# Optimization experiments

Measured on AMD Instinct MI355X. Metric: run time of the kernel, lower is better.

The kernel has to match this reference:

```python
import jax, jax.numpy as jnp
import numpy as np

N = 50000
E = 1600000
HID = 128
K = 2
EPS = 0.3


def setup_inputs() -> dict:
    key = jax.random.key(0)
    ks = jax.random.split(key, 8)
    x = jax.random.normal(ks[0], (N, 512), dtype=jnp.float32)
    edge_index = jax.random.randint(ks[1], (2, E), 0, N, dtype=jnp.int32)
    t1_w = jax.random.normal(ks[2], (HID, 512), dtype=jnp.float32) * (1.414 / np.sqrt(512))
    t1_b = jnp.zeros((HID,), dtype=jnp.float32)
    gate_w = jax.random.normal(ks[3], (K, 2 * HID), dtype=jnp.float32) * (1.414 / np.sqrt(2 * HID))
    gate_b = jnp.zeros((K,), dtype=jnp.float32)
    t2_w = jax.random.normal(ks[4], (40, HID), dtype=jnp.float32) * (1.414 / np.sqrt(HID))
    t2_b = jnp.zeros((40,), dtype=jnp.float32)
    return {"x": x, "edge_index": edge_index, "t1_w": t1_w, "t1_b": t1_b,
            "gate_w": gate_w, "gate_b": gate_b, "t2_w": t2_w, "t2_b": t2_b}


def reference(x, edge_index, t1_w, t1_b, gate_w, gate_b, t2_w, t2_b):
    row, col = edge_index[0], edge_index[1]
    # degree(row, num_nodes=N).clamp(min=1) ** -0.5
    deg = jax.ops.segment_sum(jnp.ones((E,), dtype=x.dtype), row, num_segments=N)
    norm_degree = jnp.clip(deg, 1.0) ** -0.5  # [N]

    h = jax.nn.relu(x @ t1_w.T + t1_b)  # [N, HID]
    raw = h
    for k in range(K):
        # gate(cat([h[row], h[col]], 1)) == h[row] @ W[:H] + h[col] @ W[H:]
        w_r, w_c = gate_w[k, :HID], gate_w[k, HID:]
        g = jnp.tanh(h[row] @ w_r + h[col] @ w_c + gate_b[k])  # [E]
        norm = g * norm_degree[row] * norm_degree[col]          # [E]
        # message: norm * x_j (x_j = h[row], source), scatter-add at col (target)
        agg = jax.ops.segment_sum(norm[:, None] * h[row], col, num_segments=N)
        h = EPS * raw + agg
    logits = h @ t2_w.T + t2_b  # [N, 40]
    return jax.nn.log_softmax(logits, axis=1)
```

## Files before the change

kernel.cpp:

```cpp
#include <hip/hip_runtime.h>
#include <hip/hip_bf16.h>
#include <hip/hip_fp16.h>

#define N_NODES 50000
#define N_EDGES 1600000
#define HIDDEN  128
#define EPS_C   0.3f
#define NWORDS  12500
#define CHUNK   12500
#define NCHUNK  128

typedef _Float16 f16x8 __attribute__((ext_vector_type(8)));
typedef _Float16 f16x4 __attribute__((ext_vector_type(4)));
typedef float    f32x16 __attribute__((ext_vector_type(16)));

__global__ __launch_bounds__(256) void k_hist(const int* __restrict__ ei, unsigned int* __restrict__ part) {
    __shared__ unsigned int hist[NWORDS];
    int b = blockIdx.x;
    int type  = b >> 7;
    int chunk = b & 127;
    const int* src = ei + (size_t)type * N_EDGES + (size_t)chunk * CHUNK;
    for (int i = threadIdx.x; i < NWORDS; i += 256) hist[i] = 0;
    __syncthreads();
    for (int i = threadIdx.x; i < CHUNK; i += 256) {
        int v = src[i];
        atomicAdd(&hist[v >> 2], 1u << ((v & 3) * 8));
    }
    __syncthreads();
    unsigned int* dst = part + ((size_t)type * NCHUNK + chunk) * NWORDS;
    for (int i = threadIdx.x; i < NWORDS; i += 256) dst[i] = hist[i];
}

__global__ __launch_bounds__(256) void k_reduce(const unsigned int* __restrict__ part,
                                                float* __restrict__ nd, int* __restrict__ cnt,
                                                unsigned short* __restrict__ cntpre) {
    int w = blockIdx.x * 256 + threadIdx.x;
    if (w >= NWORDS) return;
    unsigned int s0 = 0, s1 = 0, s2 = 0, s3 = 0;
    const unsigned int* dp = part + w;
    for (int b = 0; b < NCHUNK; ++b) {
        unsigned int v = dp[(size_t)b * NWORDS];
        s0 += v & 255u; s1 += (v >> 8) & 255u; s2 += (v >> 16) & 255u; s3 += v >> 24;
    }
    nd[4 * w + 0] = rsqrtf(fmaxf((float)s0, 1.f));
    nd[4 * w + 1] = rsqrtf(fmaxf((float)s1, 1.f));
    nd[4 * w + 2] = rsqrtf(fmaxf((float)s2, 1.f));
    nd[4 * w + 3] = rsqrtf(fmaxf((float)s3, 1.f));
    const unsigned int* cp = part + (size_t)NCHUNK * NWORDS + w;
    unsigned int r0 = 0, r1 = 0, r2 = 0, r3 = 0;
    for (int b = 0; b < NCHUNK; ++b) {
        size_t o = (size_t)b * N_NODES + 4 * w;
        *(ushort4*)&cntpre[o] = make_ushort4((unsigned short)r0, (unsigned short)r1,
                                             (unsigned short)r2, (unsigned short)r3);
        unsigned int v = cp[(size_t)b * NWORDS];
        r0 += v & 255u; r1 += (v >> 8) & 255u; r2 += (v >> 16) & 255u; r3 += v >> 24;
    }
    cnt[4 * w + 0] = (int)r0;
    cnt[4 * w + 1] = (int)r1;
    cnt[4 * w + 2] = (int)r2;
    cnt[4 * w + 3] = (int)r3;
}

__global__ __launch_bounds__(256) void k_scan_a(const int* __restrict__ cnt,
                                                int* __restrict__ out, int* __restrict__ partials) {
    __shared__ int sh[256];
    int t = threadIdx.x;
    int base = blockIdx.x * 1024 + t * 4;
    int v0 = (base + 0 < N_NODES) ? cnt[base + 0] : 0;
    int v1 = (base + 1 < N_NODES) ? cnt[base + 1] : 0;
    int v2 = (base + 2 < N_NODES) ? cnt[base + 2] : 0;
    int v3 = (base + 3 < N_NODES) ? cnt[base + 3] : 0;
    int s = v0 + v1 + v2 + v3;
    sh[t] = s;
    __syncthreads();
    for (int off = 1; off < 256; off <<= 1) {
        int add = (t >= off) ? sh[t - off] : 0;
        __syncthreads();
        sh[t] += add;
        __syncthreads();
    }
    int excl = sh[t] - s;
    if (t == 255) partials[blockIdx.x] = sh[255];
    if (base + 0 < N_NODES) out[base + 0] = excl;
    if (base + 1 < N_NODES) out[base + 1] = excl + v0;
    if (base + 2 < N_NODES) out[base + 2] = excl + v0 + v1;
    if (base + 3 < N_NODES) out[base + 3] = excl + v0 + v1 + v2;
}

__global__ void k_scan_b(int* partials, int* colptr, int nb) {
    if (threadIdx.x == 0 && blockIdx.x == 0) {
        int run = 0;
        for (int i = 0; i < nb; ++i) { int t = partials[i]; partials[i] = run; run += t; }
        colptr[N_NODES] = run;
    }
}

__global__ void k_scan_c(int* __restrict__ colptr, const int* __restrict__ partials) {
    int i = blockIdx.x * blockDim.x + threadIdx.x;
    if (i >= N_NODES) return;
    colptr[i] += partials[i >> 10];
}

__global__ __launch_bounds__(256) void k_scatter2(const int* __restrict__ ei, const int* __restrict__ colptr,
                                                  const unsigned short* __restrict__ cntpre,
                                                  int* __restrict__ csr) {
    __shared__ unsigned int rank[NWORDS];
    int b = blockIdx.x;
    for (int i = threadIdx.x; i < NWORDS; i += 256) rank[i] = 0;
    __syncthreads();
    const int* rs = ei + (size_t)b * CHUNK;
    const int* cs = ei + N_EDGES + (size_t)b * CHUNK;
    const unsigned short* pre = cntpre + (size_t)b * N_NODES;
    for (int i = threadIdx.x; i < CHUNK; i += 256) {
        int r = rs[i];
        int c = cs[i];
        unsigned int old = atomicAdd(&rank[c >> 2], 1u << ((c & 3) * 8));
        unsigned int lr = (old >> ((c & 3) * 8)) & 255u;
        int pos = colptr[c] + (int)pre[c] + (int)lr;
        csr[pos] = r;
    }
}

__global__ void k_cvt(const float4* __restrict__ src, __half2* __restrict__ dst, int n4) {
    int i = blockIdx.x * 256 + threadIdx.x;
    if (i >= n4) return;
    float4 v = src[i];
    dst[2 * i]     = __floats2half2_rn(v.x, v.y);
    dst[2 * i + 1] = __floats2half2_rn(v.z, v.w);
}

__global__ void k_cvtw(const float4* __restrict__ src, __half2* __restrict__ dst, int n4src, int n4tot) {
    int i = blockIdx.x * 256 + threadIdx.x;
    if (i >= n4tot) return;
    if (i < n4src) {
        float4 v = src[i];
        dst[2 * i]     = __floats2half2_rn(v.x, v.y);
        dst[2 * i + 1] = __floats2half2_rn(v.z, v.w);
    } else {
        __half2 z = __floats2half2_rn(0.f, 0.f);
        dst[2 * i]     = z;
        dst[2 * i + 1] = z;
    }
}

__global__ __launch_bounds__(256) void k_gemm1(const float* __restrict__ x, const _Float16* __restrict__ wh,
                                               const float* __restrict__ bias, _Float16* __restrict__ hb) {
    __shared__ _Float16 As[64 * 64];
    __shared__ _Float16 Bs[128 * 64];
    int t = threadIdx.x;
    int wave = t >> 6;
    int lane = t & 63;
    int lm   = lane & 31;
    int half = lane >> 5;
    int mstrip = wave & 1;
    int nstrip = wave >> 1;

    int m0  = blockIdx.x * 64;
    int wm0 = m0 + mstrip * 32;
    int n0  = nstrip * 64;

    int aidx[4], arow[4], ac4[4];
    int bidx, brow[4], bg[4];
#pragma unroll
    for (int i = 0; i < 4; ++i) {
        aidx[i] = i * 256 + t;
        arow[i] = aidx[i] >> 4;
        ac4[i]  = aidx[i] & 15;
        bidx    = i * 256 + t;
        brow[i] = bidx >> 3;
        bg[i]   = bidx & 7;
    }

    float4 pa[4];
    f16x8  pb[4];
#define LOAD_TILES(K0)                                                                    \
    {                                                                                     \
        _Pragma("unroll")                                                                 \
        for (int i = 0; i < 4; ++i) {                                                     \
            int gr = m0 + arow[i]; if (gr >= N_NODES) gr = N_NODES - 1;                   \
            pa[i] = *(const float4*)(x + (size_t)gr * 512 + (K0) + ac4[i] * 4);           \
            pb[i] = *(const f16x8*)(wh + (size_t)brow[i] * 512 + (K0) + bg[i] * 8);       \
        }                                                                                 \
    }

    f32x16 acc0, acc1;
#pragma unroll
    for (int i = 0; i < 16; ++i) { acc0[i] = 0.f; acc1[i] = 0.f; }

    int ar = mstrip * 32 + lm;
    int brA = n0 + lm;
    int brB = n0 + 32 + lm;

    LOAD_TILES(0);
    for (int k0 = 0; k0 < 512; k0 += 64) {
#pragma unroll
        for (int i = 0; i < 4; ++i) {
            f16x4 a;
            a[0] = (_Float16)pa[i].x; a[1] = (_Float16)pa[i].y;
            a[2] = (_Float16)pa[i].z; a[3] = (_Float16)pa[i].w;
            int g = ac4[i] >> 1;
            *(f16x4*)&As[arow[i] * 64 + (((g ^ (arow[i] & 7)) << 3)) + (ac4[i] & 1) * 4] = a;
            *(f16x8*)&Bs[brow[i] * 64 + ((bg[i] ^ (brow[i] & 7)) << 3)] = pb[i];
        }
        __syncthreads();
        if (k0 + 64 < 512) LOAD_TILES(k0 + 64);
#pragma unroll
        for (int kk = 0; kk < 4; ++kk) {
            int ag = kk * 2 + half;
            f16x8 av  = *(const f16x8*)&As[ar  * 64 + ((ag ^ (ar  & 7)) << 3)];
            f16x8 bv0 = *(const f16x8*)&Bs[brA * 64 + ((ag ^ (brA & 7)) << 3)];
            f16x8 bv1 = *(const f16x8*)&Bs[brB * 64 + ((ag ^ (brA & 7)) << 3)];
            acc0 = __builtin_amdgcn_mfma_f32_32x32x16_f16(av, bv0, acc0, 0, 0, 0);
            acc1 = __builtin_amdgcn_mfma_f32_32x32x16_f16(av, bv1, acc1, 0, 0, 0);
        }
        __syncthreads();
    }
#undef LOAD_TILES

    float bs0 = bias[n0 + lm];
    float bs1 = bias[n0 + 32 + lm];
#pragma unroll
    for (int reg = 0; reg < 16; ++reg) {
        int row = (reg & 3) + 8 * (reg >> 2) + 4 * half;
        int gm = wm0 + row;
        if (gm < N_NODES) {
            float v0 = fmaxf(acc0[reg] + bs0, 0.f);
            float v1 = fmaxf(acc1[reg] + bs1, 0.f);
            hb[(size_t)gm * HIDDEN + n0 + lm]      = (_Float16)v0;
            hb[(size_t)gm * HIDDEN + n0 + 32 + lm] = (_Float16)v1;
        }
    }
}

__global__ __launch_bounds__(256) void k_dot(const __half2* __restrict__ hb, const float* __restrict__ gw,
                                             const float* __restrict__ gb, const float* __restrict__ nd,
                                             int layer, float2* __restrict__ dn, float* __restrict__ dcb) {
    int node = blockIdx.x * 4 + (threadIdx.x >> 6);
    int lane = threadIdx.x & 63;
    if (node >= N_NODES) return;
    float2 wr = ((const float2*)(gw + layer * 256))[lane];
    float2 wc = ((const float2*)(gw + layer * 256 + 128))[lane];
    float2 hc = __half22float2(hb[(size_t)node * 64 + lane]);
    float a = hc.x * wr.x + hc.y * wr.y;
    float b = hc.x * wc.x + hc.y * wc.y;
#pragma unroll
    for (int off = 32; off >= 1; off >>= 1) {
        a += __shfl_xor(a, off, 64);
        b += __shfl_xor(b, off, 64);
    }
    if (lane == 0) {
        dn[node]  = make_float2(a, nd[node]);
        dcb[node] = b + gb[layer];
    }
}

__global__ __launch_bounds__(256) void k_edgew(const int* __restrict__ csr, const int* __restrict__ colptr,
                                               const float2* __restrict__ dn, const float* __restrict__ dcb,
                                               float* __restrict__ warr) {
    int node = blockIdx.x * 8 + (threadIdx.x >> 5);
    int sl   = threadIdx.x & 31;
    if (node >= N_NODES) return;
    float dc  = dcb[node];
    int beg = colptr[node], end = colptr[node + 1];
    for (int p = beg + sl; p < end; p += 32) {
        int r = csr[p];
        float2 v = dn[r];
        float xx = v.x + dc;
        float t = __expf(2.0f * xx);
        float g = 1.0f - 2.0f / (t + 1.0f);
        warr[p] = g * v.y;
    }
}

__global__ __launch_bounds__(256) void k_prop(const __half2* __restrict__ hb, const __half2* __restrict__ rawh,
                                              const int* __restrict__ colptr, const int* __restrict__ csr,
                                              const float* __restrict__ warr, const float* __restrict__ nd,
                                              const float* __restrict__ gw_next, const float* __restrict__ gb_next,
                                              float2* __restrict__ dn, float* __restrict__ dcb,
                                              __half2* __restrict__ hbn) {
    int lane = threadIdx.x & 63;
    int node = __builtin_amdgcn_readfirstlane(blockIdx.x * 4 + (threadIdx.x >> 6));
    int beg = __builtin_amdgcn_readfirstlane(colptr[node]);
    int end = __builtin_amdgcn_readfirstlane(colptr[node + 1]);
    float acc0 = 0.f, acc1 = 0.f;
    int p = beg;
    for (; p + 8 <= end; p += 8) {
        int r0 = csr[p + 0], r1 = csr[p + 1], r2 = csr[p + 2], r3 = csr[p + 3];
        int r4 = csr[p + 4], r5 = csr[p + 5], r6 = csr[p + 6], r7 = csr[p + 7];
        float w0 = warr[p + 0], w1 = warr[p + 1], w2 = warr[p + 2], w3 = warr[p + 3];
        float w4 = warr[p + 4], w5 = warr[p + 5], w6 = warr[p + 6], w7 = warr[p + 7];
        __half2 v0 = hb[(size_t)r0 * 64 + lane];
        __half2 v1 = hb[(size_t)r1 * 64 + lane];
        __half2 v2 = hb[(size_t)r2 * 64 + lane];
        __half2 v3 = hb[(size_t)r3 * 64 + lane];
        __half2 v4 = hb[(size_t)r4 * 64 + lane];
        __half2 v5 = hb[(size_t)r5 * 64 + lane];
        __half2 v6 = hb[(size_t)r6 * 64 + lane];
        __half2 v7 = hb[(size_t)r7 * 64 + lane];
        acc0 = fmaf(w0, __low2float(v0), acc0);  acc1 = fmaf(w0, __high2float(v0), acc1);
        acc0 = fmaf(w1, __low2float(v1), acc0);  acc1 = fmaf(w1, __high2float(v1), acc1);
        acc0 = fmaf(w2, __low2float(v2), acc0);  acc1 = fmaf(w2, __high2float(v2), acc1);
        acc0 = fmaf(w3, __low2float(v3), acc0);  acc1 = fmaf(w3, __high2float(v3), acc1);
        acc0 = fmaf(w4, __low2float(v4), acc0);  acc1 = fmaf(w4, __high2float(v4), acc1);
        acc0 = fmaf(w5, __low2float(v5), acc0);  acc1 = fmaf(w5, __high2float(v5), acc1);
        acc0 = fmaf(w6, __low2float(v6), acc0);  acc1 = fmaf(w6, __high2float(v6), acc1);
        acc0 = fmaf(w7, __low2float(v7), acc0);  acc1 = fmaf(w7, __high2float(v7), acc1);
    }
    for (; p < end; ++p) {
        int r = csr[p];
        float w = warr[p];
        __half2 v = hb[(size_t)r * 64 + lane];
        acc0 = fmaf(w, __low2float(v), acc0);
        acc1 = fmaf(w, __high2float(v), acc1);
    }
    float ndc = nd[node];
    float2 rw = __half22float2(rawh[(size_t)node * 64 + lane]);
    float2 o;
    o.x = fmaf(EPS_C, rw.x, ndc * acc0);
    o.y = fmaf(EPS_C, rw.y, ndc * acc1);
    hbn[(size_t)node * 64 + lane] = __floats2half2_rn(o.x, o.y);
    if (gw_next) {
        float2 wr = ((const float2*)gw_next)[lane];
        float2 wc = ((const float2*)(gw_next + 128))[lane];
        float a = o.x * wr.x + o.y * wr.y;
        float b = o.x * wc.x + o.y * wc.y;
#pragma unroll
        for (int off = 32; off >= 1; off >>= 1) {
            a += __shfl_xor(a, off, 64);
            b += __shfl_xor(b, off, 64);
        }
        if (lane == 0) {
            dn[node]  = make_float2(a, ndc);
            dcb[node] = b + gb_next[0];
        }
    }
}

__global__ __launch_bounds__(256) void k_out(const _Float16* __restrict__ h16, const _Float16* __restrict__ w2h,
                                             const float* __restrict__ b2, float* __restrict__ out) {
    int wave = threadIdx.x >> 6;
    int lane = threadIdx.x & 63;
    int lm   = lane & 31;
    int half = lane >> 5;

    int wm0 = blockIdx.x * 128 + wave * 32;
    int m   = wm0 + lm;
    int mc  = (m < N_NODES) ? m : (N_NODES - 1);

    const _Float16* arow  = h16 + (size_t)mc * HIDDEN + half * 8;
    const _Float16* brow0 = w2h + (size_t)lm * HIDDEN + half * 8;
    const _Float16* brow1 = w2h + (size_t)(32 + lm) * HIDDEN + half * 8;

    f32x16 acc0, acc1;
#pragma unroll
    for (int i = 0; i < 16; ++i) { acc0[i] = 0.f; acc1[i] = 0.f; }

#pragma unroll
    for (int k0 = 0; k0 < 128; k0 += 16) {
        f16x8 av = *(const f16x8*)(arow  + k0);
        f16x8 b0 = *(const f16x8*)(brow0 + k0);
        f16x8 b1 = *(const f16x8*)(brow1 + k0);
        acc0 = __builtin_amdgcn_mfma_f32_32x32x16_f16(av, b0, acc0, 0, 0, 0);
        acc1 = __builtin_amdgcn_mfma_f32_32x32x16_f16(av, b1, acc1, 0, 0, 0);
    }

    float bj0 = b2[lm];
    float bj1 = (lm < 8) ? b2[32 + lm] : 0.f;

#pragma unroll
    for (int reg = 0; reg < 16; ++reg) {
        int row = (reg & 3) + 8 * (reg >> 2) + 4 * half;
        float v0 = acc0[reg] + bj0;
        float v1 = (lm < 8) ? (acc1[reg] + bj1) : -INFINITY;
        float mx = fmaxf(v0, v1);
#pragma unroll
        for (int off = 16; off >= 1; off >>= 1) mx = fmaxf(mx, __shfl_xor(mx, off, 64));
        float s = __expf(v0 - mx) + ((lm < 8) ? __expf(v1 - mx) : 0.f);
#pragma unroll
        for (int off = 16; off >= 1; off >>= 1) s += __shfl_xor(s, off, 64);
        float ls = __logf(s) + mx;
        int gm = wm0 + row;
        if (gm < N_NODES) {
            out[(size_t)gm * 40 + lm] = v0 - ls;
            if (lm < 8) out[(size_t)gm * 40 + 32 + lm] = v1 - ls;
        }
    }
}

extern "C" void kernel_launch(void* const* d_in, const int* in_sizes, int n_in,
                              void* d_out, int out_size, void* d_ws, size_t ws_size,
                              hipStream_t stream) {
    const float* x   = (const float*)d_in[0];
    const int*   ei  = (const int*)  d_in[1];
    const float* t1w = (const float*)d_in[2];
    const float* t1b = (const float*)d_in[3];
    const float* gw  = (const float*)d_in[4];
    const float* gb  = (const float*)d_in[5];
    const float* w2  = (const float*)d_in[6];
    const float* b2  = (const float*)d_in[7];
    float* out = (float*)d_out;

    char* p = (char*)d_ws;
    int*    colptr   = (int*)p;    p += (size_t)(N_NODES + 64) * 4;
    int*    partials = (int*)p;    p += 256 * 4;
    float*  nd       = (float*)p;  p += (size_t)N_NODES * 4;
    int*    cnt      = (int*)p;    p += (size_t)N_NODES * 4;
    float*  dcb      = (float*)p;  p += (size_t)N_NODES * 4;
    float2* dn       = (float2*)p; p += (size_t)N_NODES * 8;
    int*    csr      = (int*)p;    p += (size_t)N_EDGES * 4;
    float*  warr     = (float*)p;  p += (size_t)N_EDGES * 4;
    _Float16* wh     = (_Float16*)p; p += (size_t)HIDDEN * 512 * 2;
    _Float16* w2h    = (_Float16*)p; p += (size_t)64 * HIDDEN * 2;
    char* q = p;
    unsigned int*   part   = (unsigned int*)q;
    unsigned short* cntpre = (unsigned short*)(q + (size_t)2 * NCHUNK * NWORDS * 4);
    __half2* hb0 = (__half2*)p; p += (size_t)N_NODES * 64 * 4;
    __half2* hb1 = (__half2*)p; p += (size_t)N_NODES * 64 * 4;
    __half2* hb2 = (__half2*)p; p += (size_t)N_NODES * 64 * 4;

    k_hist<<<2 * NCHUNK, 256, 0, stream>>>(ei, part);
    k_reduce<<<(NWORDS + 255) / 256, 256, 0, stream>>>(part, nd, cnt, cntpre);
    int nb = (N_NODES + 1023) / 1024;
    k_scan_a<<<nb, 256, 0, stream>>>(cnt, colptr, partials);
    k_scan_b<<<1, 64, 0, stream>>>(partials, colptr, nb);
    k_scan_c<<<(N_NODES + 255) / 256, 256, 0, stream>>>(colptr, partials);
    k_scatter2<<<NCHUNK, 256, 0, stream>>>(ei, colptr, cntpre, csr);

    k_cvt<<<(16384 + 255) / 256, 256, 0, stream>>>((const float4*)t1w, (__half2*)wh, 16384);
    k_cvtw<<<8, 256, 0, stream>>>((const float4*)w2, (__half2*)w2h, 40 * HIDDEN / 4, 64 * HIDDEN / 4);
    k_gemm1<<<(N_NODES + 63) / 64, 256, 0, stream>>>(x, wh, t1b, (_Float16*)hb0);

    k_dot  <<<(N_NODES + 3) / 4, 256, 0, stream>>>(hb0, gw, gb, nd, 0, dn, dcb);
    k_edgew<<<(N_NODES + 7) / 8, 256, 0, stream>>>(csr, colptr, dn, dcb, warr);
    k_prop <<<(N_NODES + 3) / 4, 256, 0, stream>>>(hb0, hb0, colptr, csr, warr, nd,
                                                   gw + 256, gb + 1, dn, dcb, hb1);

    k_edgew<<<(N_NODES + 7) / 8, 256, 0, stream>>>(csr, colptr, dn, dcb, warr);
    k_prop <<<(N_NODES + 3) / 4, 256, 0, stream>>>(hb1, hb0, colptr, csr, warr, nd,
                                                   (const float*)nullptr, (const float*)nullptr,
                                                   (float2*)nullptr, (float*)nullptr, hb2);

    k_out<<<(N_NODES + 127) / 128, 256, 0, stream>>>((const _Float16*)hb2, w2h, b2, out);
}
```

Before: 450.9 us.

## Fuse edge-weight computation into propagation kernel and shrink prefix counts to bytes

Removes the separate k_edgew pass and its 1.6M-entry weight array. Each wave now computes up to 64 edge gate weights cooperatively, stages them with source indices in shared memory, and then gathers neighbor features. The per-layer dn/dcb buffers are double-buffered so the fused kernel can read the current layer's values while writing the next. The per-chunk prefix count array is narrowed from 16-bit to 8-bit, which halves its traffic but would overflow if a node's count within one chunk prefix reaches 256. The shared-memory staging relies on wave-synchronous execution with no barrier, and padded tail entries get zero weight.

```diff
diff --git a/kernel.cpp b/kernel.cpp
--- a/kernel.cpp
+++ b/kernel.cpp
@@ -33,7 +33,7 @@
 
 __global__ __launch_bounds__(256) void k_reduce(const unsigned int* __restrict__ part,
                                                 float* __restrict__ nd, int* __restrict__ cnt,
-                                                unsigned short* __restrict__ cntpre) {
+                                                unsigned char* __restrict__ cntpre) {
     int w = blockIdx.x * 256 + threadIdx.x;
     if (w >= NWORDS) return;
     unsigned int s0 = 0, s1 = 0, s2 = 0, s3 = 0;
@@ -50,8 +50,8 @@
     unsigned int r0 = 0, r1 = 0, r2 = 0, r3 = 0;
     for (int b = 0; b < NCHUNK; ++b) {
         size_t o = (size_t)b * N_NODES + 4 * w;
-        *(ushort4*)&cntpre[o] = make_ushort4((unsigned short)r0, (unsigned short)r1,
-                                             (unsigned short)r2, (unsigned short)r3);
+        *(uchar4*)&cntpre[o] = make_uchar4((unsigned char)r0, (unsigned char)r1,
+                                           (unsigned char)r2, (unsigned char)r3);
         unsigned int v = cp[(size_t)b * NWORDS];
         r0 += v & 255u; r1 += (v >> 8) & 255u; r2 += (v >> 16) & 255u; r3 += v >> 24;
     }
@@ -102,7 +102,7 @@
 }
 
 __global__ __launch_bounds__(256) void k_scatter2(const int* __restrict__ ei, const int* __restrict__ colptr,
-                                                  const unsigned short* __restrict__ cntpre,
+                                                  const unsigned char* __restrict__ cntpre,
                                                   int* __restrict__ csr) {
     __shared__ unsigned int rank[NWORDS];
     int b = blockIdx.x;
@@ -110,7 +110,7 @@
     __syncthreads();
     const int* rs = ei + (size_t)b * CHUNK;
     const int* cs = ei + N_EDGES + (size_t)b * CHUNK;
-    const unsigned short* pre = cntpre + (size_t)b * N_NODES;
+    const unsigned char* pre = cntpre + (size_t)b * N_NODES;
     for (int i = threadIdx.x; i < CHUNK; i += 256) {
         int r = rs[i];
         int c = cs[i];
@@ -254,64 +254,57 @@
     }
 }
 
-__global__ __launch_bounds__(256) void k_edgew(const int* __restrict__ csr, const int* __restrict__ colptr,
-                                               const float2* __restrict__ dn, const float* __restrict__ dcb,
-                                               float* __restrict__ warr) {
-    int node = blockIdx.x * 8 + (threadIdx.x >> 5);
-    int sl   = threadIdx.x & 31;
-    if (node >= N_NODES) return;
-    float dc  = dcb[node];
-    int beg = colptr[node], end = colptr[node + 1];
-    for (int p = beg + sl; p < end; p += 32) {
-        int r = csr[p];
-        float2 v = dn[r];
+__global__ __launch_bounds__(256) void k_prop(const __half2* __restrict__ hb, const __half2* __restrict__ rawh,
+                                              const int* __restrict__ colptr, const int* __restrict__ csr,
+                                              const float2* __restrict__ dn_in, const float* __restrict__ dcb_in,
+                                              const float* __restrict__ nd,
+                                              const float* __restrict__ gw_next, const float* __restrict__ gb_next,
+                                              float2* __restrict__ dn_out, float* __restrict__ dcb_out,
+                                              __half2* __restrict__ hbn) {
+    __shared__ int   lrs[4][64];
+    __shared__ float lws[4][64];
+    int lane = threadIdx.x & 63;
+    int wid  = threadIdx.x >> 6;
+    int node = __builtin_amdgcn_readfirstlane(blockIdx.x * 4 + wid);
+    int beg = __builtin_amdgcn_readfirstlane(colptr[node]);
+    int end = __builtin_amdgcn_readfirstlane(colptr[node + 1]);
+    float dc = dcb_in[node];
+    float acc0 = 0.f, acc1 = 0.f;
+    for (int base = beg; base < end; base += 64) {
+        int e  = base + lane;
+        int ec = (e < end) ? e : (end - 1);
+        int r  = csr[ec];
+        float2 v = dn_in[r];
         float xx = v.x + dc;
         float t = __expf(2.0f * xx);
         float g = 1.0f - 2.0f / (t + 1.0f);
-        warr[p] = g * v.y;
-    }
-}
-
-__global__ __launch_bounds__(256) void k_prop(const __half2* __restrict__ hb, const __half2* __restrict__ rawh,
-                                              const int* __restrict__ colptr, const int* __restrict__ csr,
-                                              const float* __restrict__ warr, const float* __restrict__ nd,
-                                              const float* __restrict__ gw_next, const float* __restrict__ gb_next,
-                                              float2* __restrict__ dn, float* __restrict__ dcb,
-                                              __half2* __restrict__ hbn) {
-    int lane = threadIdx.x & 63;
-    int node = __builtin_amdgcn_readfirstlane(blockIdx.x * 4 + (threadIdx.x >> 6));
-    int beg = __builtin_amdgcn_readfirstlane(colptr[node]);
-    int end = __builtin_amdgcn_readfirstlane(colptr[node + 1]);
-    float acc0 = 0.f, acc1 = 0.f;
-    int p = beg;
-    for (; p + 8 <= end; p += 8) {
-        int r0 = csr[p + 0], r1 = csr[p + 1], r2 = csr[p + 2], r3 = csr[p + 3];
-        int r4 = csr[p + 4], r5 = csr[p + 5], r6 = csr[p + 6], r7 = csr[p + 7];
-        float w0 = warr[p + 0], w1 = warr[p + 1], w2 = warr[p + 2], w3 = warr[p + 3];
-        float w4 = warr[p + 4], w5 = warr[p + 5], w6 = warr[p + 6], w7 = warr[p + 7];
-        __half2 v0 = hb[(size_t)r0 * 64 + lane];
-        __half2 v1 = hb[(size_t)r1 * 64 + lane];
-        __half2 v2 = hb[(size_t)r2 * 64 + lane];
-        __half2 v3 = hb[(size_t)r3 * 64 + lane];
-        __half2 v4 = hb[(size_t)r4 * 64 + lane];
-        __half2 v5 = hb[(size_t)r5 * 64 + lane];
-        __half2 v6 = hb[(size_t)r6 * 64 + lane];
-        __half2 v7 = hb[(size_t)r7 * 64 + lane];
-        acc0 = fmaf(w0, __low2float(v0), acc0);  acc1 = fmaf(w0, __high2float(v0), acc1);
-        acc0 = fmaf(w1, __low2float(v1), acc0);  acc1 = fmaf(w1, __high2float(v1), acc1);
-        acc0 = fmaf(w2, __low2float(v2), acc0);  acc1 = fmaf(w2, __high2float(v2), acc1);
-        acc0 = fmaf(w3, __low2float(v3), acc0);  acc1 = fmaf(w3, __high2float(v3), acc1);
-        acc0 = fmaf(w4, __low2float(v4), acc0);  acc1 = fmaf(w4, __high2float(v4), acc1);
-        acc0 = fmaf(w5, __low2float(v5), acc0);  acc1 = fmaf(w5, __high2float(v5), acc1);
-        acc0 = fmaf(w6, __low2float(v6), acc0);  acc1 = fmaf(w6, __high2float(v6), acc1);
-        acc0 = fmaf(w7, __low2float(v7), acc0);  acc1 = fmaf(w7, __high2float(v7), acc1);
-    }
-    for (; p < end; ++p) {
-        int r = csr[p];
-        float w = warr[p];
-        __half2 v = hb[(size_t)r * 64 + lane];
-        acc0 = fmaf(w, __low2float(v), acc0);
-        acc1 = fmaf(w, __high2float(v), acc1);
+        float w = (e < end) ? g * v.y : 0.f;
+        lrs[wid][lane] = r;
+        lws[wid][lane] = w;
+        int m = end - base; if (m > 64) m = 64;
+        int mm = (m + 7) & ~7;
+        for (int j = 0; j < mm; j += 8) {
+            int r0 = lrs[wid][j + 0], r1 = lrs[wid][j + 1], r2 = lrs[wid][j + 2], r3 = lrs[wid][j + 3];
+            int r4 = lrs[wid][j + 4], r5 = lrs[wid][j + 5], r6 = lrs[wid][j + 6], r7 = lrs[wid][j + 7];
+            float w0 = lws[wid][j + 0], w1 = lws[wid][j + 1], w2 = lws[wid][j + 2], w3 = lws[wid][j + 3];
+            float w4 = lws[wid][j + 4], w5 = lws[wid][j + 5], w6 = lws[wid][j + 6], w7 = lws[wid][j + 7];
+            __half2 v0 = hb[(size_t)r0 * 64 + lane];
+            __half2 v1 = hb[(size_t)r1 * 64 + lane];
+            __half2 v2 = hb[(size_t)r2 * 64 + lane];
+            __half2 v3 = hb[(size_t)r3 * 64 + lane];
+            __half2 v4 = hb[(size_t)r4 * 64 + lane];
+            __half2 v5 = hb[(size_t)r5 * 64 + lane];
+            __half2 v6 = hb[(size_t)r6 * 64 + lane];
+            __half2 v7 = hb[(size_t)r7 * 64 + lane];
+            acc0 = fmaf(w0, __low2float(v0), acc0);  acc1 = fmaf(w0, __high2float(v0), acc1);
+            acc0 = fmaf(w1, __low2float(v1), acc0);  acc1 = fmaf(w1, __high2float(v1), acc1);
+            acc0 = fmaf(w2, __low2float(v2), acc0);  acc1 = fmaf(w2, __high2float(v2), acc1);
+            acc0 = fmaf(w3, __low2float(v3), acc0);  acc1 = fmaf(w3, __high2float(v3), acc1);
+            acc0 = fmaf(w4, __low2float(v4), acc0);  acc1 = fmaf(w4, __high2float(v4), acc1);
+            acc0 = fmaf(w5, __low2float(v5), acc0);  acc1 = fmaf(w5, __high2float(v5), acc1);
+            acc0 = fmaf(w6, __low2float(v6), acc0);  acc1 = fmaf(w6, __high2float(v6), acc1);
+            acc0 = fmaf(w7, __low2float(v7), acc0);  acc1 = fmaf(w7, __high2float(v7), acc1);
+        }
     }
     float ndc = nd[node];
     float2 rw = __half22float2(rawh[(size_t)node * 64 + lane]);
@@ -330,8 +323,8 @@
             b += __shfl_xor(b, off, 64);
         }
         if (lane == 0) {
-            dn[node]  = make_float2(a, ndc);
-            dcb[node] = b + gb_next[0];
+            dn_out[node]  = make_float2(a, ndc);
+            dcb_out[node] = b + gb_next[0];
         }
     }
 }
@@ -405,15 +398,16 @@
     int*    partials = (int*)p;    p += 256 * 4;
     float*  nd       = (float*)p;  p += (size_t)N_NODES * 4;
     int*    cnt      = (int*)p;    p += (size_t)N_NODES * 4;
-    float*  dcb      = (float*)p;  p += (size_t)N_NODES * 4;
-    float2* dn       = (float2*)p; p += (size_t)N_NODES * 8;
+    float*  dcb0     = (float*)p;  p += (size_t)N_NODES * 4;
+    float*  dcb1     = (float*)p;  p += (size_t)N_NODES * 4;
+    float2* dn0      = (float2*)p; p += (size_t)N_NODES * 8;
+    float2* dn1      = (float2*)p; p += (size_t)N_NODES * 8;
     int*    csr      = (int*)p;    p += (size_t)N_EDGES * 4;
-    float*  warr     = (float*)p;  p += (size_t)N_EDGES * 4;
     _Float16* wh     = (_Float16*)p; p += (size_t)HIDDEN * 512 * 2;
     _Float16* w2h    = (_Float16*)p; p += (size_t)64 * HIDDEN * 2;
     char* q = p;
-    unsigned int*   part   = (unsigned int*)q;
-    unsigned short* cntpre = (unsigned short*)(q + (size_t)2 * NCHUNK * NWORDS * 4);
+    unsigned int*  part   = (unsigned int*)q;
+    unsigned char* cntpre = (unsigned char*)(q + (size_t)2 * NCHUNK * NWORDS * 4);
     __half2* hb0 = (__half2*)p; p += (size_t)N_NODES * 64 * 4;
     __half2* hb1 = (__half2*)p; p += (size_t)N_NODES * 64 * 4;
     __half2* hb2 = (__half2*)p; p += (size_t)N_NODES * 64 * 4;
@@ -430,15 +424,12 @@
     k_cvtw<<<8, 256, 0, stream>>>((const float4*)w2, (__half2*)w2h, 40 * HIDDEN / 4, 64 * HIDDEN / 4);
     k_gemm1<<<(N_NODES + 63) / 64, 256, 0, stream>>>(x, wh, t1b, (_Float16*)hb0);
 
-    k_dot  <<<(N_NODES + 3) / 4, 256, 0, stream>>>(hb0, gw, gb, nd, 0, dn, dcb);
-    k_edgew<<<(N_NODES + 7) / 8, 256, 0, stream>>>(csr, colptr, dn, dcb, warr);
-    k_prop <<<(N_NODES + 3) / 4, 256, 0, stream>>>(hb0, hb0, colptr, csr, warr, nd,
-                                                   gw + 256, gb + 1, dn, dcb, hb1);
-
-    k_edgew<<<(N_NODES + 7) / 8, 256, 0, stream>>>(csr, colptr, dn, dcb, warr);
-    k_prop <<<(N_NODES + 3) / 4, 256, 0, stream>>>(hb1, hb0, colptr, csr, warr, nd,
-                                                   (const float*)nullptr, (const float*)nullptr,
-                                                   (float2*)nullptr, (float*)nullptr, hb2);
+    k_dot<<<(N_NODES + 3) / 4, 256, 0, stream>>>(hb0, gw, gb, nd, 0, dn0, dcb0);
+    k_prop<<<(N_NODES + 3) / 4, 256, 0, stream>>>(hb0, hb0, colptr, csr, dn0, dcb0, nd,
+                                                  gw + 256, gb + 1, dn1, dcb1, hb1);
+    k_prop<<<(N_NODES + 3) / 4, 256, 0, stream>>>(hb1, hb0, colptr, csr, dn1, dcb1, nd,
+                                                  (const float*)nullptr, (const float*)nullptr,
+                                                  (float2*)nullptr, (float*)nullptr, hb2);
 
     k_out<<<(N_NODES + 127) / 128, 256, 0, stream>>>((const _Float16*)hb2, w2h, b2, out);
 }
```

Measured after the change: 449.3 us. No clear change (-0.4%).
